# Kernel tuning notes

Measured on AMD Instinct MI355X. Metric: run time of the kernel, lower is better.

The kernel has to match this reference:

```python
import jax, jax.numpy as jnp
import numpy as np

B, L, IN, H, T = 512, 16, 128, 1024, 64


def setup_inputs() -> dict:
    key = jax.random.key(0)
    ks = jax.random.split(key, 11)
    k = 1.0 / np.sqrt(H)  # torch default init scale
    u = lambda kk, shape: jax.random.uniform(kk, shape, jnp.float32, -k, k)
    return {
        "x": jax.random.normal(ks[0], (B, L, IN), jnp.float32),
        "W_ih0": u(ks[1], (4 * H, IN)),
        "W_hh0": u(ks[2], (4 * H, H)),
        "b_ih0": u(ks[3], (4 * H,)),
        "b_hh0": u(ks[4], (4 * H,)),
        "W_ih1": u(ks[5], (4 * H, H)),
        "W_hh1": u(ks[6], (4 * H, H)),
        "b_ih1": u(ks[7], (4 * H,)),
        "b_hh1": u(ks[8], (4 * H,)),
        "W_out": u(ks[9], (IN, H)),
        "b_out": u(ks[10], (IN,)),
        "t": T,
    }


def _cell(xt, h, c, W_ih, W_hh, b_ih, b_hh):
    # PyTorch LSTM cell; gate order i, f, g, o
    g = xt @ W_ih.T + h @ W_hh.T + (b_ih + b_hh)
    i, f, gg, o = jnp.split(g, 4, axis=-1)
    c = jax.nn.sigmoid(f) * c + jax.nn.sigmoid(i) * jnp.tanh(gg)
    h = jax.nn.sigmoid(o) * jnp.tanh(c)
    return h, c


def reference(x, W_ih0, W_hh0, b_ih0, b_hh0, W_ih1, W_hh1, b_ih1, b_hh1,
              W_out, b_out, t):
    layers = ((W_ih0, W_hh0, b_ih0, b_hh0), (W_ih1, W_hh1, b_ih1, b_hh1))
    Bn = x.shape[0]
    Hn = W_hh0.shape[1]

    def stack_step(state, xt):
        new_state = []
        inp = xt
        for (h, c), p in zip(state, layers):
            h, c = _cell(inp, h, c, *p)
            new_state.append((h, c))
            inp = h
        return tuple(new_state), inp  # inp = top-layer hidden [B, H]

    z = jnp.zeros((Bn, Hn), x.dtype)
    state0 = tuple((z, z) for _ in layers)

    # prompt phase: process x over time, keep final state and last top hidden
    state, tops = jax.lax.scan(stack_step, state0, x.transpose(1, 0, 2))
    x_last = x[:, -1] + (tops[-1] @ W_out.T + b_out)  # [B, IN]

    def gen_step(carry, _):
        st, xl = carry
        st, htop = stack_step(st, xl)
        xl = xl + (htop @ W_out.T + b_out)
        return (st, xl), xl

    (_, _), gen = jax.lax.scan(gen_step, (state, x_last), None, length=t - 1)

    out = jnp.concatenate(
        [x, x_last[:, None, :], gen.transpose(1, 0, 2)], axis=1
    )  # [B, L + t, IN]
    return out
```

## Files before the change

### kernel.cpp

```cpp
#include <hip/hip_runtime.h>

#define B_    512
#define L_    16
#define IN_   128
#define H_    1024
#define T_    64
#define OUTROW 10240

#define LDC   1040
#define LDXL  144
#define RSTRIDE 67

#define KH_X  64
#define KH_H  32
#define KH_XL 4
#define KH_W0 36
#define KH_W1 64
#define KH_WO 32

typedef __attribute__((ext_vector_type(8))) short bf8;
typedef __attribute__((ext_vector_type(4))) float f4;
typedef __attribute__((ext_vector_type(4))) unsigned short us4;
typedef unsigned short u16;
typedef unsigned int   u32;

#define MFMA16(a, b, c) __builtin_amdgcn_mfma_f32_16x16x32_bf16(a, b, c, 0, 0, 0)

__device__ __forceinline__ u16 f2bf(float f) {
    u32 u = __builtin_bit_cast(u32, f);
    u32 r = (u + 0x7fffu + ((u >> 16) & 1u)) >> 16;
    return (u16)r;
}
__device__ __forceinline__ float sigm(float x) { return 1.f / (1.f + __expf(-x)); }
__device__ __forceinline__ float tanh_f(float x) {
    float ax = fabsf(x);
    float e = __expf(-2.f * ax);
    float t = (1.f - e) / (1.f + e);
    return x < 0.f ? -t : t;
}
__device__ __forceinline__ bf8 ld8(const u16* p) { return *(const bf8*)p; }

__device__ __forceinline__ size_t swz(int kh_stride, int row, int k) {
    return ((size_t)(row >> 4) * kh_stride + (k >> 5)) * 512
           + ((k & 31) >> 3) * 128 + (row & 15) * 8 + (k & 7);
}

#define MFMAT(AS, BS)                                                       \
  do {                                                                      \
    _Pragma("unroll")                                                       \
    for (int s_ = 0; s_ < 2; ++s_)                                          \
      _Pragma("unroll")                                                     \
      for (int g_ = 0; g_ < 4; ++g_)                                        \
        _Pragma("unroll")                                                   \
        for (int t_ = 0; t_ < 4; ++t_)                                      \
          acc[g_][t_] = MFMA16(AS[s_ * 4 + g_], BS[s_ * 4 + t_], acc[g_][t_]); \
  } while (0)

#define LOADT_CELL(AS, BS, KT)                                              \
  do {                                                                      \
    const int kt_ = (KT);                                                   \
    const bool ix_ = kt_ < nk1;                                             \
    const int khA_ = (ix_ ? kt_ : kt_ - nk1) * 2;                           \
    const int khB_ = kt_ * 2;                                               \
    _Pragma("unroll")                                                       \
    for (int s_ = 0; s_ < 2; ++s_) {                                        \
      _Pragma("unroll")                                                     \
      for (int g_ = 0; g_ < 4; ++g_)                                        \
        AS[s_ * 4 + g_] = ld8((ix_ ? apx[g_] : aph[g_]) + (khA_ + s_) * 512); \
      _Pragma("unroll")                                                     \
      for (int t_ = 0; t_ < 4; ++t_)                                        \
        BS[s_ * 4 + t_] = ld8(bp[t_] + (khB_ + s_) * 512);                  \
    }                                                                       \
  } while (0)

#define LOADT_PROJ(AS, BS, KT)                                              \
  do {                                                                      \
    const int kh_ = (KT) * 2;                                               \
    _Pragma("unroll")                                                       \
    for (int s_ = 0; s_ < 2; ++s_) {                                        \
      _Pragma("unroll")                                                     \
      for (int g_ = 0; g_ < 4; ++g_)                                        \
        AS[s_ * 4 + g_] = ld8(ap[g_] + (kh_ + s_) * 512);                   \
      _Pragma("unroll")                                                     \
      for (int t_ = 0; t_ < 4; ++t_)                                        \
        BS[s_ * 4 + t_] = ld8(bp[t_] + (kh_ + s_) * 512);                   \
    }                                                                       \
  } while (0)

__global__ __launch_bounds__(256, 2) void cell_gemm(
    const u16* __restrict__ pA0, int kh0, int nk1,
    const u16* __restrict__ pA1, int kh1, int nk2,
    const u16* __restrict__ pB, int khB,
    const float* __restrict__ bias, float* __restrict__ Cst, u16* __restrict__ Hdst)
{
    __shared__ float red[4][64 * RSTRIDE];
    const int bid = blockIdx.x;
    const int tn = (bid & 7) * 8 + ((bid >> 3) & 7);
    const int tm = bid >> 6;
    const int tid = threadIdx.x;
    const int lane = tid & 63, ws = tid >> 6;
    const int l15 = lane & 15, qd = lane >> 4, q4 = qd * 4;

    const int erow = ws * 16 + l15;
    const int grow = tm * 64 + erow;
    const int colb = tn * 16 + q4;
    const f4 cold = *(const f4*)&Cst[(size_t)grow * LDC + colb];

    f4 acc[4][4];
#pragma unroll
    for (int i = 0; i < 4; ++i)
#pragma unroll
        for (int j = 0; j < 4; ++j) acc[i][j] = (f4)(0.f);

    const u16* bp[4];
#pragma unroll
    for (int t = 0; t < 4; ++t)
        bp[t] = pB + (size_t)(tn * 4 + t) * khB * 512 + lane * 8;
    const u16* apx[4];
    const u16* aph[4];
#pragma unroll
    for (int g = 0; g < 4; ++g) {
        apx[g] = pA0 + (size_t)(tm * 4 + g) * kh0 * 512 + lane * 8;
        aph[g] = pA1 + (size_t)(tm * 4 + g) * kh1 * 512 + lane * 8;
    }

    const int nk  = nk1 + nk2;
    const int myn = (nk - ws + 3) >> 2;

    bf8 A0[8], B0[8], A1[8], B1[8];
    LOADT_CELL(A0, B0, ws);
    int i = 0, kt = ws;
    for (; i + 2 <= myn; i += 2, kt += 8) {
        LOADT_CELL(A1, B1, kt + 4);
        MFMAT(A0, B0);
        if (i + 2 < myn) LOADT_CELL(A0, B0, kt + 8);
        MFMAT(A1, B1);
    }
    if (i < myn) MFMAT(A0, B0);

#pragma unroll
    for (int rg = 0; rg < 4; ++rg)
#pragma unroll
        for (int t = 0; t < 4; ++t)
#pragma unroll
            for (int r = 0; r < 4; ++r)
                red[ws][(rg * 16 + q4 + r) * RSTRIDE + t * 16 + l15] = acc[rg][t][r];
    __syncthreads();

    f4 gs[4];
#pragma unroll
    for (int G = 0; G < 4; ++G) {
        f4 s;
#pragma unroll
        for (int j = 0; j < 4; ++j) {
            const int cidx = erow * RSTRIDE + G * 16 + q4 + j;
            s[j] = red[0][cidx] + red[1][cidx] + red[2][cidx] + red[3][cidx];
        }
        gs[G] = s + *(const f4*)&bias[tn * 64 + G * 16 + q4];
    }
    f4 cn; us4 h4;
#pragma unroll
    for (int j = 0; j < 4; ++j) {
        const float I  = sigm(gs[0][j]);
        const float F  = sigm(gs[1][j]);
        const float Gg = tanh_f(gs[2][j]);
        const float O  = sigm(gs[3][j]);
        cn[j] = F * cold[j] + I * Gg;
        h4[j] = f2bf(O * tanh_f(cn[j]));
    }
    *(f4*)&Cst[(size_t)grow * LDC + colb] = cn;
    *(us4*)&Hdst[swz(KH_H, grow, colb)] = h4;
}

__global__ __launch_bounds__(256, 2) void proj_gemm(
    const u16* __restrict__ pA,
    const u16* __restrict__ pB,
    const float* __restrict__ bout,
    const float* __restrict__ xin, int ldxin,
    float* __restrict__ XL, u16* __restrict__ XLbf,
    float* __restrict__ dout, int slot)
{
    __shared__ float red[4][64 * RSTRIDE];
    const int bid = blockIdx.x;
    const int tn = bid >> 3, tm = bid & 7;
    const int tid = threadIdx.x;
    const int lane = tid & 63, ws = tid >> 6;
    const int l15 = lane & 15, qd = lane >> 4;

    f4 acc[4][4];
#pragma unroll
    for (int i = 0; i < 4; ++i)
#pragma unroll
        for (int j = 0; j < 4; ++j) acc[i][j] = (f4)(0.f);

    const u16* bp[4];
#pragma unroll
    for (int t = 0; t < 4; ++t)
        bp[t] = pB + (size_t)(tn * 4 + t) * KH_WO * 512 + lane * 8;
    const u16* ap[4];
#pragma unroll
    for (int g = 0; g < 4; ++g)
        ap[g] = pA + (size_t)(tm * 4 + g) * KH_H * 512 + lane * 8;

    const int myn = 4;
    bf8 A0[8], B0[8], A1[8], B1[8];
    LOADT_PROJ(A0, B0, ws);
    int i = 0, kt = ws;
    for (; i + 2 <= myn; i += 2, kt += 8) {
        LOADT_PROJ(A1, B1, kt + 4);
        MFMAT(A0, B0);
        if (i + 2 < myn) LOADT_PROJ(A0, B0, kt + 8);
        MFMAT(A1, B1);
    }

#pragma unroll
    for (int rg = 0; rg < 4; ++rg)
#pragma unroll
        for (int t = 0; t < 4; ++t)
#pragma unroll
            for (int r = 0; r < 4; ++r)
                red[ws][(rg * 16 + qd * 4 + r) * RSTRIDE + t * 16 + l15] = acc[rg][t][r];
    __syncthreads();

    const int erow = ws * 16 + l15;
    const int grow = tm * 64 + erow;
#pragma unroll
    for (int jb = 0; jb < 4; ++jb) {
        const int cin = qd * 16 + jb * 4;
        const int col = tn * 64 + cin;
        f4 s;
#pragma unroll
        for (int j2 = 0; j2 < 4; ++j2) {
            const int cidx = erow * RSTRIDE + cin + j2;
            s[j2] = red[0][cidx] + red[1][cidx] + red[2][cidx] + red[3][cidx];
        }
        const f4 v = *(const f4*)&xin[(size_t)grow * ldxin + col] + s
                     + *(const f4*)&bout[col];
        *(f4*)&XL[(size_t)grow * LDXL + col] = v;
        us4 b;
#pragma unroll
        for (int j2 = 0; j2 < 4; ++j2) b[j2] = f2bf(v[j2]);
        *(us4*)&XLbf[swz(KH_XL, grow, col)] = b;
        *(f4*)&dout[(size_t)grow * OUTROW + slot * IN_ + col] = v;
    }
}

__global__ void conv_w(const float* Wih0, const float* Whh0, const float* bih0, const float* bhh0,
                       const float* Wih1, const float* Whh1, const float* bih1, const float* bhh1,
                       const float* Wout,
                       u16* W0c, float* b0p, u16* W1c, float* b1p, u16* Woutb)
{
    const int bid = blockIdx.x, t = threadIdx.x;
    const int lane = t >> 2;
    const int l15 = lane & 15, qd = lane >> 4;
    const int j0 = (t & 3) * 2;
    const int c0_ = qd * 8 + j0;

    if (bid < 9216) {
        const int rg = bid / 36, kh = bid - rg * 36;
        const int p = rg * 16 + l15;
        const int rem = p & 63, G = rem >> 4, u = (p >> 6) * 16 + (rem & 15);
        const int src = G * H_ + u;
        float e0, e1;
        if (kh < 4) {
            e0 = Wih0[(size_t)src * IN_ + kh * 32 + c0_];
            e1 = Wih0[(size_t)src * IN_ + kh * 32 + c0_ + 1];
        } else {
            e0 = Whh0[(size_t)src * H_ + (kh - 4) * 32 + c0_];
            e1 = Whh0[(size_t)src * H_ + (kh - 4) * 32 + c0_ + 1];
        }
        ((u32*)W0c)[(size_t)bid * 256 + t] = (u32)f2bf(e0) | ((u32)f2bf(e1) << 16);
        if (kh == 0 && qd == 0 && j0 == 0) b0p[p] = bih0[src] + bhh0[src];
    } else if (bid < 25600) {
        const int x = bid - 9216;
        const int rg = x >> 6, kh = x & 63;
        const int p = rg * 16 + l15;
        const int rem = p & 63, G = rem >> 4, u = (p >> 6) * 16 + (rem & 15);
        const int src = G * H_ + u;
        float e0, e1;
        if (kh < 32) {
            e0 = Wih1[(size_t)src * H_ + kh * 32 + c0_];
            e1 = Wih1[(size_t)src * H_ + kh * 32 + c0_ + 1];
        } else {
            e0 = Whh1[(size_t)src * H_ + (kh - 32) * 32 + c0_];
            e1 = Whh1[(size_t)src * H_ + (kh - 32) * 32 + c0_ + 1];
        }
        ((u32*)W1c)[(size_t)x * 256 + t] = (u32)f2bf(e0) | ((u32)f2bf(e1) << 16);
        if (kh == 0 && qd == 0 && j0 == 0) b1p[p] = bih1[src] + bhh1[src];
    } else {
        const int x = bid - 25600;
        const int rg = x >> 5, kh = x & 31;
        const int r = rg * 16 + l15;
        const float e0 = Wout[(size_t)r * H_ + kh * 32 + c0_];
        const float e1 = Wout[(size_t)r * H_ + kh * 32 + c0_ + 1];
        ((u32*)Woutb)[(size_t)x * 256 + t] = (u32)f2bf(e0) | ((u32)f2bf(e1) << 16);
    }
}

__global__ void setup_k(const float* __restrict__ x, u16* __restrict__ Xb,
                        u16* H0, u16* H1, float* c0, float* c1,
                        float* __restrict__ dout)
{
    const int i = blockIdx.x * 256 + threadIdx.x;
    const float v = x[i];
    const int r = i >> 11, col = i & 2047;
    Xb[swz(KH_X, r, col)] = f2bf(v);
    dout[(size_t)r * OUTROW + col] = v;
    if (i < B_ * H_) {
        H0[i] = 0; H1[i] = 0;
        const int rr = i >> 10, cc = i & 1023;
        c0[(size_t)rr * LDC + cc] = 0.f; c1[(size_t)rr * LDC + cc] = 0.f;
    }
}

extern "C" void kernel_launch(void* const* d_in, const int* in_sizes, int n_in,
                              void* d_out, int out_size, void* d_ws, size_t ws_size,
                              hipStream_t stream)
{
    const float* x    = (const float*)d_in[0];
    const float* Wih0 = (const float*)d_in[1];
    const float* Whh0 = (const float*)d_in[2];
    const float* bih0 = (const float*)d_in[3];
    const float* bhh0 = (const float*)d_in[4];
    const float* Wih1 = (const float*)d_in[5];
    const float* Whh1 = (const float*)d_in[6];
    const float* bih1 = (const float*)d_in[7];
    const float* bhh1 = (const float*)d_in[8];
    const float* Wout = (const float*)d_in[9];
    const float* bout = (const float*)d_in[10];
    float* dout = (float*)d_out;

    char* ws = (char*)d_ws;
    size_t off = 0;
    auto alloc = [&](size_t bytes) -> char* {
        char* p = ws + off; off += (bytes + 255) & ~(size_t)255; return p;
    };
    u16*  W0c   = (u16*)alloc((size_t)9216 * 1024);
    u16*  W1c   = (u16*)alloc((size_t)16384 * 1024);
    u16*  Woutb = (u16*)alloc((size_t)256 * 1024);
    float* b0p  = (float*)alloc(4096 * 4);
    float* b1p  = (float*)alloc(4096 * 4);
    u16*  Xb    = (u16*)alloc((size_t)2048 * 1024);
    u16*  H0b[2]; H0b[0] = (u16*)alloc((size_t)1024 * 1024); H0b[1] = (u16*)alloc((size_t)1024 * 1024);
    u16*  H1b[2]; H1b[0] = (u16*)alloc((size_t)1024 * 1024); H1b[1] = (u16*)alloc((size_t)1024 * 1024);
    float* c0   = (float*)alloc((size_t)B_ * LDC * 4);
    float* c1   = (float*)alloc((size_t)B_ * LDC * 4);
    float* XL   = (float*)alloc((size_t)B_ * LDXL * 4);
    u16*  XLbf  = (u16*)alloc((size_t)128 * 1024);

    conv_w<<<25856, 256, 0, stream>>>(Wih0, Whh0, bih0, bhh0,
                                      Wih1, Whh1, bih1, bhh1, Wout,
                                      W0c, b0p, W1c, b1p, Woutb);
    setup_k<<<4096, 256, 0, stream>>>(x, Xb, H0b[0], H1b[0], c0, c1, dout);

    int p = 0;
    for (int g = 0; g < 79; ++g) {
        const u16* xpart; int khx;
        if (g < 16) { xpart = Xb + (size_t)g * 2048; khx = KH_X; }
        else        { xpart = XLbf;                  khx = KH_XL; }
        cell_gemm<<<512, 256, 0, stream>>>(xpart, khx, 2, H0b[p], KH_H, 16,
                                           W0c, KH_W0, b0p, c0, H0b[1 - p]);
        cell_gemm<<<512, 256, 0, stream>>>(H0b[1 - p], KH_H, 16, H1b[p], KH_H, 16,
                                           W1c, KH_W1, b1p, c1, H1b[1 - p]);
        if (g >= 15) {
            const int s = g - 15;
            const float* xin; int ldxin;
            if (s == 0) { xin = x + 15 * IN_; ldxin = L_ * IN_; }
            else        { xin = XL;           ldxin = LDXL; }
            proj_gemm<<<16, 256, 0, stream>>>(H1b[1 - p], Woutb, bout,
                                              xin, ldxin, XL, XLbf, dout, 16 + s);
        }
        p ^= 1;
    }
}
```

Measured before the change: 2.676 ms.

## Wavefront-pair prompt LSTM layers and widen cell blocks to eight waves

During the prompt phase, layer 1 at step g and layer 0 at step g+1 are independent, so they now run as one combined launch of 1024 blocks. This doubles the parallelism per launch and cuts the launch count. Cell and projection kernels move to 512 threads (8 waves splitting K), with template-specialised strides. The LDS reduction runs in two rounds with a per-element epilogue. The software double-buffered register prefetch is removed, which relies on higher occupancy to hide memory latency, and the reduction now has more LDS traffic and an extra barrier.

```diff
diff --git a/kernel.cpp b/kernel.cpp
--- a/kernel.cpp
+++ b/kernel.cpp
@@ -9,7 +9,7 @@
 
 #define LDC   1040
 #define LDXL  144
-#define RSTRIDE 67
+#define RST   68
 
 #define KH_X  64
 #define KH_H  32
@@ -45,201 +45,195 @@
            + ((k & 31) >> 3) * 128 + (row & 15) * 8 + (k & 7);
 }
 
-#define MFMAT(AS, BS)                                                       \
-  do {                                                                      \
-    _Pragma("unroll")                                                       \
-    for (int s_ = 0; s_ < 2; ++s_)                                          \
-      _Pragma("unroll")                                                     \
-      for (int g_ = 0; g_ < 4; ++g_)                                        \
-        _Pragma("unroll")                                                   \
-        for (int t_ = 0; t_ < 4; ++t_)                                      \
-          acc[g_][t_] = MFMA16(AS[s_ * 4 + g_], BS[s_ * 4 + t_], acc[g_][t_]); \
-  } while (0)
-
-#define LOADT_CELL(AS, BS, KT)                                              \
-  do {                                                                      \
-    const int kt_ = (KT);                                                   \
-    const bool ix_ = kt_ < nk1;                                             \
-    const int khA_ = (ix_ ? kt_ : kt_ - nk1) * 2;                           \
-    const int khB_ = kt_ * 2;                                               \
-    _Pragma("unroll")                                                       \
-    for (int s_ = 0; s_ < 2; ++s_) {                                        \
-      _Pragma("unroll")                                                     \
-      for (int g_ = 0; g_ < 4; ++g_)                                        \
-        AS[s_ * 4 + g_] = ld8((ix_ ? apx[g_] : aph[g_]) + (khA_ + s_) * 512); \
-      _Pragma("unroll")                                                     \
-      for (int t_ = 0; t_ < 4; ++t_)                                        \
-        BS[s_ * 4 + t_] = ld8(bp[t_] + (khB_ + s_) * 512);                  \
-    }                                                                       \
-  } while (0)
-
-#define LOADT_PROJ(AS, BS, KT)                                              \
-  do {                                                                      \
-    const int kh_ = (KT) * 2;                                               \
-    _Pragma("unroll")                                                       \
-    for (int s_ = 0; s_ < 2; ++s_) {                                        \
-      _Pragma("unroll")                                                     \
-      for (int g_ = 0; g_ < 4; ++g_)                                        \
-        AS[s_ * 4 + g_] = ld8(ap[g_] + (kh_ + s_) * 512);                   \
-      _Pragma("unroll")                                                     \
-      for (int t_ = 0; t_ < 4; ++t_)                                        \
-        BS[s_ * 4 + t_] = ld8(bp[t_] + (kh_ + s_) * 512);                   \
-    }                                                                       \
-  } while (0)
-
-__global__ __launch_bounds__(256, 2) void cell_gemm(
-    const u16* __restrict__ pA0, int kh0, int nk1,
-    const u16* __restrict__ pA1, int kh1, int nk2,
-    const u16* __restrict__ pB, int khB,
-    const float* __restrict__ bias, float* __restrict__ Cst, u16* __restrict__ Hdst)
-{
-    __shared__ float red[4][64 * RSTRIDE];
-    const int bid = blockIdx.x;
+template<int KH0, int NK1, int KH1, int NK2, int KHB>
+__device__ __forceinline__ void gemm_loop(f4 (&acc)[4][4], int tm, int tn,
+    int lane, int ws,
+    const u16* __restrict__ pA0, const u16* __restrict__ pA1,
+    const u16* __restrict__ pB)
+{
+#pragma unroll
+    for (int i = 0; i < 4; ++i)
+#pragma unroll
+        for (int j = 0; j < 4; ++j) acc[i][j] = (f4)(0.f);
+
+    const int lo = lane * 8;
+    const int nk  = NK1 + NK2;
+    const int myn = (nk - ws + 7) >> 3;
+
+    bf8 A[4], B[4];
+    for (int m = 0; m < myn; ++m) {
+        const int kt = ws + m * 8;
+        const bool ix = kt < NK1;
+        const int khA = (ix ? kt : kt - NK1) * 2;
+        const int khB = kt * 2;
+        const u16* ap = ix ? pA0 : pA1;
+        const int khs = ix ? KH0 : KH1;
+#pragma unroll
+        for (int s = 0; s < 2; ++s) {
+#pragma unroll
+            for (int g = 0; g < 4; ++g)
+                A[g] = ld8(ap + ((size_t)(tm * 4 + g) * khs + khA + s) * 512 + lo);
+#pragma unroll
+            for (int t = 0; t < 4; ++t)
+                B[t] = ld8(pB + ((size_t)(tn * 4 + t) * KHB + khB + s) * 512 + lo);
+#pragma unroll
+            for (int g = 0; g < 4; ++g)
+#pragma unroll
+                for (int t = 0; t < 4; ++t)
+                    acc[g][t] = MFMA16(A[g], B[t], acc[g][t]);
+        }
+    }
+}
+
+template<int KH0, int NK1, int KH1, int NK2, int KHB>
+__device__ __forceinline__ void cell_body(int bid,
+    const u16* __restrict__ pA0, const u16* __restrict__ pA1,
+    const u16* __restrict__ pB, const float* __restrict__ bias,
+    float* __restrict__ Cst, u16* __restrict__ Hdst, float* red)
+{
     const int tn = (bid & 7) * 8 + ((bid >> 3) & 7);
     const int tm = bid >> 6;
     const int tid = threadIdx.x;
     const int lane = tid & 63, ws = tid >> 6;
-    const int l15 = lane & 15, qd = lane >> 4, q4 = qd * 4;
-
-    const int erow = ws * 16 + l15;
-    const int grow = tm * 64 + erow;
-    const int colb = tn * 16 + q4;
-    const f4 cold = *(const f4*)&Cst[(size_t)grow * LDC + colb];
+    const int l15 = lane & 15, qd = lane >> 4;
+
+    const int eu = tid & 15, elr = tid >> 4;
+    const int ecol = tn * 16 + eu;
+    const float cold0 = Cst[(size_t)(tm * 64 + elr) * LDC + ecol];
+    const float cold1 = Cst[(size_t)(tm * 64 + 32 + elr) * LDC + ecol];
+    f4 bi;
+#pragma unroll
+    for (int G = 0; G < 4; ++G) bi[G] = bias[tn * 64 + G * 16 + eu];
 
     f4 acc[4][4];
-#pragma unroll
-    for (int i = 0; i < 4; ++i)
-#pragma unroll
-        for (int j = 0; j < 4; ++j) acc[i][j] = (f4)(0.f);
-
-    const u16* bp[4];
-#pragma unroll
-    for (int t = 0; t < 4; ++t)
-        bp[t] = pB + (size_t)(tn * 4 + t) * khB * 512 + lane * 8;
-    const u16* apx[4];
-    const u16* aph[4];
-#pragma unroll
-    for (int g = 0; g < 4; ++g) {
-        apx[g] = pA0 + (size_t)(tm * 4 + g) * kh0 * 512 + lane * 8;
-        aph[g] = pA1 + (size_t)(tm * 4 + g) * kh1 * 512 + lane * 8;
-    }
-
-    const int nk  = nk1 + nk2;
-    const int myn = (nk - ws + 3) >> 2;
-
-    bf8 A0[8], B0[8], A1[8], B1[8];
-    LOADT_CELL(A0, B0, ws);
-    int i = 0, kt = ws;
-    for (; i + 2 <= myn; i += 2, kt += 8) {
-        LOADT_CELL(A1, B1, kt + 4);
-        MFMAT(A0, B0);
-        if (i + 2 < myn) LOADT_CELL(A0, B0, kt + 8);
-        MFMAT(A1, B1);
-    }
-    if (i < myn) MFMAT(A0, B0);
-
-#pragma unroll
-    for (int rg = 0; rg < 4; ++rg)
-#pragma unroll
-        for (int t = 0; t < 4; ++t)
-#pragma unroll
-            for (int r = 0; r < 4; ++r)
-                red[ws][(rg * 16 + q4 + r) * RSTRIDE + t * 16 + l15] = acc[rg][t][r];
-    __syncthreads();
-
-    f4 gs[4];
-#pragma unroll
-    for (int G = 0; G < 4; ++G) {
-        f4 s;
-#pragma unroll
-        for (int j = 0; j < 4; ++j) {
-            const int cidx = erow * RSTRIDE + G * 16 + q4 + j;
-            s[j] = red[0][cidx] + red[1][cidx] + red[2][cidx] + red[3][cidx];
-        }
-        gs[G] = s + *(const f4*)&bias[tn * 64 + G * 16 + q4];
-    }
-    f4 cn; us4 h4;
-#pragma unroll
-    for (int j = 0; j < 4; ++j) {
-        const float I  = sigm(gs[0][j]);
-        const float F  = sigm(gs[1][j]);
-        const float Gg = tanh_f(gs[2][j]);
-        const float O  = sigm(gs[3][j]);
-        cn[j] = F * cold[j] + I * Gg;
-        h4[j] = f2bf(O * tanh_f(cn[j]));
-    }
-    *(f4*)&Cst[(size_t)grow * LDC + colb] = cn;
-    *(us4*)&Hdst[swz(KH_H, grow, colb)] = h4;
-}
-
-__global__ __launch_bounds__(256, 2) void proj_gemm(
-    const u16* __restrict__ pA,
-    const u16* __restrict__ pB,
+    gemm_loop<KH0, NK1, KH1, NK2, KHB>(acc, tm, tn, lane, ws, pA0, pA1, pB);
+
+#pragma unroll
+    for (int round = 0; round < 2; ++round) {
+        if (round) __syncthreads();
+#pragma unroll
+        for (int rh = 0; rh < 2; ++rh) {
+            const int rg = round * 2 + rh;
+#pragma unroll
+            for (int t = 0; t < 4; ++t)
+#pragma unroll
+                for (int r = 0; r < 4; ++r)
+                    red[ws * (32 * RST) + (rh * 16 + qd * 4 + r) * RST + t * 16 + l15]
+                        = acc[rg][t][r];
+        }
+        __syncthreads();
+
+        float g4[4];
+#pragma unroll
+        for (int G = 0; G < 4; ++G) {
+            float s = 0.f;
+#pragma unroll
+            for (int w = 0; w < 8; ++w)
+                s += red[w * (32 * RST) + elr * RST + G * 16 + eu];
+            g4[G] = s + bi[G];
+        }
+        const float I  = sigm(g4[0]);
+        const float F  = sigm(g4[1]);
+        const float Gg = tanh_f(g4[2]);
+        const float O  = sigm(g4[3]);
+        const int grow = tm * 64 + round * 32 + elr;
+        const float cn = F * (round ? cold1 : cold0) + I * Gg;
+        Cst[(size_t)grow * LDC + ecol] = cn;
+        Hdst[swz(KH_H, grow, ecol)] = f2bf(O * tanh_f(cn));
+    }
+}
+
+__global__ __launch_bounds__(512, 4) void cell_prompt0(
+    const u16* __restrict__ pA0, const u16* __restrict__ pA1,
+    const u16* __restrict__ pB, const float* __restrict__ bias,
+    float* __restrict__ Cst, u16* __restrict__ Hdst)
+{
+    __shared__ float red[8 * 32 * RST];
+    cell_body<KH_X, 2, KH_H, 16, KH_W0>(blockIdx.x, pA0, pA1, pB, bias, Cst, Hdst, red);
+}
+
+__global__ __launch_bounds__(512, 4) void cell_roll0(
+    const u16* __restrict__ pA0, const u16* __restrict__ pA1,
+    const u16* __restrict__ pB, const float* __restrict__ bias,
+    float* __restrict__ Cst, u16* __restrict__ Hdst)
+{
+    __shared__ float red[8 * 32 * RST];
+    cell_body<KH_XL, 2, KH_H, 16, KH_W0>(blockIdx.x, pA0, pA1, pB, bias, Cst, Hdst, red);
+}
+
+__global__ __launch_bounds__(512, 4) void cell_l1(
+    const u16* __restrict__ pA0, const u16* __restrict__ pA1,
+    const u16* __restrict__ pB, const float* __restrict__ bias,
+    float* __restrict__ Cst, u16* __restrict__ Hdst)
+{
+    __shared__ float red[8 * 32 * RST];
+    cell_body<KH_H, 16, KH_H, 16, KH_W1>(blockIdx.x, pA0, pA1, pB, bias, Cst, Hdst, red);
+}
+
+__global__ __launch_bounds__(512, 4) void pair_k(
+    const u16* __restrict__ A0a, const u16* __restrict__ A1a,
+    const u16* __restrict__ Ba, const float* __restrict__ ba,
+    float* __restrict__ Ca, u16* __restrict__ Ha,
+    const u16* __restrict__ A0b, const u16* __restrict__ A1b,
+    const u16* __restrict__ Bb, const float* __restrict__ bb,
+    float* __restrict__ Cb, u16* __restrict__ Hb)
+{
+    __shared__ float red[8 * 32 * RST];
+    if (blockIdx.x < 512)
+        cell_body<KH_H, 16, KH_H, 16, KH_W1>(blockIdx.x, A0a, A1a, Ba, ba, Ca, Ha, red);
+    else
+        cell_body<KH_X, 2, KH_H, 16, KH_W0>(blockIdx.x - 512, A0b, A1b, Bb, bb, Cb, Hb, red);
+}
+
+__global__ __launch_bounds__(512, 4) void proj_gemm(
+    const u16* __restrict__ pA, const u16* __restrict__ pB,
     const float* __restrict__ bout,
     const float* __restrict__ xin, int ldxin,
     float* __restrict__ XL, u16* __restrict__ XLbf,
     float* __restrict__ dout, int slot)
 {
-    __shared__ float red[4][64 * RSTRIDE];
+    __shared__ float red[8 * 32 * RST];
     const int bid = blockIdx.x;
     const int tn = bid >> 3, tm = bid & 7;
     const int tid = threadIdx.x;
     const int lane = tid & 63, ws = tid >> 6;
     const int l15 = lane & 15, qd = lane >> 4;
 
+    const int elr = tid >> 4;
+    const int c4  = (tid & 15) * 4;
+    const int col = tn * 64 + c4;
+    const f4 bo  = *(const f4*)&bout[col];
+    const f4 xv0 = *(const f4*)&xin[(size_t)(tm * 64 + elr) * ldxin + col];
+    const f4 xv1 = *(const f4*)&xin[(size_t)(tm * 64 + 32 + elr) * ldxin + col];
+
     f4 acc[4][4];
-#pragma unroll
-    for (int i = 0; i < 4; ++i)
-#pragma unroll
-        for (int j = 0; j < 4; ++j) acc[i][j] = (f4)(0.f);
-
-    const u16* bp[4];
-#pragma unroll
-    for (int t = 0; t < 4; ++t)
-        bp[t] = pB + (size_t)(tn * 4 + t) * KH_WO * 512 + lane * 8;
-    const u16* ap[4];
-#pragma unroll
-    for (int g = 0; g < 4; ++g)
-        ap[g] = pA + (size_t)(tm * 4 + g) * KH_H * 512 + lane * 8;
-
-    const int myn = 4;
-    bf8 A0[8], B0[8], A1[8], B1[8];
-    LOADT_PROJ(A0, B0, ws);
-    int i = 0, kt = ws;
-    for (; i + 2 <= myn; i += 2, kt += 8) {
-        LOADT_PROJ(A1, B1, kt + 4);
-        MFMAT(A0, B0);
-        if (i + 2 < myn) LOADT_PROJ(A0, B0, kt + 8);
-        MFMAT(A1, B1);
-    }
-
-#pragma unroll
-    for (int rg = 0; rg < 4; ++rg)
-#pragma unroll
-        for (int t = 0; t < 4; ++t)
-#pragma unroll
-            for (int r = 0; r < 4; ++r)
-                red[ws][(rg * 16 + qd * 4 + r) * RSTRIDE + t * 16 + l15] = acc[rg][t][r];
-    __syncthreads();
-
-    const int erow = ws * 16 + l15;
-    const int grow = tm * 64 + erow;
-#pragma unroll
-    for (int jb = 0; jb < 4; ++jb) {
-        const int cin = qd * 16 + jb * 4;
-        const int col = tn * 64 + cin;
-        f4 s;
-#pragma unroll
-        for (int j2 = 0; j2 < 4; ++j2) {
-            const int cidx = erow * RSTRIDE + cin + j2;
-            s[j2] = red[0][cidx] + red[1][cidx] + red[2][cidx] + red[3][cidx];
-        }
-        const f4 v = *(const f4*)&xin[(size_t)grow * ldxin + col] + s
-                     + *(const f4*)&bout[col];
+    gemm_loop<KH_H, 16, KH_H, 0, KH_WO>(acc, tm, tn, lane, ws, pA, pA, pB);
+
+#pragma unroll
+    for (int round = 0; round < 2; ++round) {
+        if (round) __syncthreads();
+#pragma unroll
+        for (int rh = 0; rh < 2; ++rh) {
+            const int rg = round * 2 + rh;
+#pragma unroll
+            for (int t = 0; t < 4; ++t)
+#pragma unroll
+                for (int r = 0; r < 4; ++r)
+                    red[ws * (32 * RST) + (rh * 16 + qd * 4 + r) * RST + t * 16 + l15]
+                        = acc[rg][t][r];
+        }
+        __syncthreads();
+
+        f4 s = (f4)(0.f);
+#pragma unroll
+        for (int w = 0; w < 8; ++w)
+            s += *(const f4*)&red[w * (32 * RST) + elr * RST + c4];
+        const f4 v = (round ? xv1 : xv0) + s + bo;
+        const int grow = tm * 64 + round * 32 + elr;
         *(f4*)&XL[(size_t)grow * LDXL + col] = v;
         us4 b;
 #pragma unroll
-        for (int j2 = 0; j2 < 4; ++j2) b[j2] = f2bf(v[j2]);
+        for (int j = 0; j < 4; ++j) b[j] = f2bf(v[j]);
         *(us4*)&XLbf[swz(KH_XL, grow, col)] = b;
         *(f4*)&dout[(size_t)grow * OUTROW + slot * IN_ + col] = v;
     }
@@ -354,22 +348,24 @@
     setup_k<<<4096, 256, 0, stream>>>(x, Xb, H0b[0], H1b[0], c0, c1, dout);
 
     int p = 0;
-    for (int g = 0; g < 79; ++g) {
-        const u16* xpart; int khx;
-        if (g < 16) { xpart = Xb + (size_t)g * 2048; khx = KH_X; }
-        else        { xpart = XLbf;                  khx = KH_XL; }
-        cell_gemm<<<512, 256, 0, stream>>>(xpart, khx, 2, H0b[p], KH_H, 16,
-                                           W0c, KH_W0, b0p, c0, H0b[1 - p]);
-        cell_gemm<<<512, 256, 0, stream>>>(H0b[1 - p], KH_H, 16, H1b[p], KH_H, 16,
-                                           W1c, KH_W1, b1p, c1, H1b[1 - p]);
-        if (g >= 15) {
-            const int s = g - 15;
-            const float* xin; int ldxin;
-            if (s == 0) { xin = x + 15 * IN_; ldxin = L_ * IN_; }
-            else        { xin = XL;           ldxin = LDXL; }
-            proj_gemm<<<16, 256, 0, stream>>>(H1b[1 - p], Woutb, bout,
-                                              xin, ldxin, XL, XLbf, dout, 16 + s);
-        }
+    cell_prompt0<<<512, 512, 0, stream>>>(Xb, H0b[0], W0c, b0p, c0, H0b[1]);
+    for (int g = 0; g < 15; ++g) {
+        pair_k<<<1024, 512, 0, stream>>>(
+            H0b[1 - p], H1b[p], W1c, b1p, c1, H1b[1 - p],
+            Xb + (size_t)(g + 1) * 2048, H0b[1 - p], W0c, b0p, c0, H0b[p]);
         p ^= 1;
     }
-}
+    cell_l1<<<512, 512, 0, stream>>>(H0b[0], H1b[1], W1c, b1p, c1, H1b[0]);
+    proj_gemm<<<16, 512, 0, stream>>>(H1b[0], Woutb, bout,
+                                      x + 15 * IN_, L_ * IN_, XL, XLbf, dout, 16);
+
+    p = 0;
+    for (int g = 16; g < 79; ++g) {
+        cell_roll0<<<512, 512, 0, stream>>>(XLbf, H0b[p], W0c, b0p, c0, H0b[1 - p]);
+        cell_l1<<<512, 512, 0, stream>>>(H0b[1 - p], H1b[p], W1c, b1p, c1, H1b[1 - p]);
+        const int s = g - 15;
+        proj_gemm<<<16, 512, 0, stream>>>(H1b[1 - p], Woutb, bout,
+                                          XL, LDXL, XL, XLbf, dout, 16 + s);
+        p ^= 1;
+    }
+}
```

Result: slower. 3.490 ms (+30.4%).

## Wavefront-pair layer0/layer1 cells in prompt phase and deepen load pipeline

Applied to the files above, without the earlier changes.

During the 16-step prompt phase, layer-1 at step t and layer-0 at step t+1 are independent, so they are fused into one 1024-block launch (pair_k). This halves the number of dependent launches in that phase and fills more CUs per launch. Separately, the GEMM inner loops are restructured from a two-stage double buffer of 8-fragment tiles into a four-stage ring of 4-fragment half-tiles, adding prefetch depth at similar register cost. The H buffer ping-pong indexing is rearranged to match the skewed schedule, which carries some correctness risk.

```diff
diff --git a/kernel.cpp b/kernel.cpp
--- a/kernel.cpp
+++ b/kernel.cpp
@@ -10,6 +10,7 @@
 #define LDC   1040
 #define LDXL  144
 #define RSTRIDE 67
+#define RSZ   (64 * RSTRIDE)
 
 #define KH_X  64
 #define KH_H  32
@@ -45,56 +46,46 @@
            + ((k & 31) >> 3) * 128 + (row & 15) * 8 + (k & 7);
 }
 
-#define MFMAT(AS, BS)                                                       \
+#define MFMAP(AS, BS)                                                       \
   do {                                                                      \
     _Pragma("unroll")                                                       \
-    for (int s_ = 0; s_ < 2; ++s_)                                          \
-      _Pragma("unroll")                                                     \
-      for (int g_ = 0; g_ < 4; ++g_)                                        \
-        _Pragma("unroll")                                                   \
-        for (int t_ = 0; t_ < 4; ++t_)                                      \
-          acc[g_][t_] = MFMA16(AS[s_ * 4 + g_], BS[s_ * 4 + t_], acc[g_][t_]); \
-  } while (0)
-
-#define LOADT_CELL(AS, BS, KT)                                              \
-  do {                                                                      \
-    const int kt_ = (KT);                                                   \
-    const bool ix_ = kt_ < nk1;                                             \
-    const int khA_ = (ix_ ? kt_ : kt_ - nk1) * 2;                           \
-    const int khB_ = kt_ * 2;                                               \
-    _Pragma("unroll")                                                       \
-    for (int s_ = 0; s_ < 2; ++s_) {                                        \
-      _Pragma("unroll")                                                     \
-      for (int g_ = 0; g_ < 4; ++g_)                                        \
-        AS[s_ * 4 + g_] = ld8((ix_ ? apx[g_] : aph[g_]) + (khA_ + s_) * 512); \
+    for (int g_ = 0; g_ < 4; ++g_)                                          \
       _Pragma("unroll")                                                     \
       for (int t_ = 0; t_ < 4; ++t_)                                        \
-        BS[s_ * 4 + t_] = ld8(bp[t_] + (khB_ + s_) * 512);                  \
-    }                                                                       \
+        acc[g_][t_] = MFMA16(AS[g_], BS[t_], acc[g_][t_]);                  \
   } while (0)
 
-#define LOADT_PROJ(AS, BS, KT)                                              \
+#define LOADP_CELL(AS, BS, PH)                                              \
   do {                                                                      \
-    const int kh_ = (KT) * 2;                                               \
+    const int kt_ = ws + (((PH) >> 1) << 2);                                \
+    const int s_  = (PH) & 1;                                               \
+    const bool ix_ = kt_ < nk1;                                             \
+    const int oA_ = (((ix_ ? kt_ : kt_ - nk1) << 1) + s_) * 512;            \
+    const int oB_ = ((kt_ << 1) + s_) * 512;                                \
     _Pragma("unroll")                                                       \
-    for (int s_ = 0; s_ < 2; ++s_) {                                        \
-      _Pragma("unroll")                                                     \
-      for (int g_ = 0; g_ < 4; ++g_)                                        \
-        AS[s_ * 4 + g_] = ld8(ap[g_] + (kh_ + s_) * 512);                   \
-      _Pragma("unroll")                                                     \
-      for (int t_ = 0; t_ < 4; ++t_)                                        \
-        BS[s_ * 4 + t_] = ld8(bp[t_] + (kh_ + s_) * 512);                   \
-    }                                                                       \
+    for (int g_ = 0; g_ < 4; ++g_)                                          \
+      AS[g_] = ld8((ix_ ? apx[g_] : aph[g_]) + oA_);                        \
+    _Pragma("unroll")                                                       \
+    for (int t_ = 0; t_ < 4; ++t_) BS[t_] = ld8(bp[t_] + oB_);              \
   } while (0)
 
-__global__ __launch_bounds__(256, 2) void cell_gemm(
+#define LOADP_PROJ(AS, BS, PH)                                              \
+  do {                                                                      \
+    const int kt_ = ws + (((PH) >> 1) << 2);                                \
+    const int o_  = ((kt_ << 1) + ((PH) & 1)) * 512;                        \
+    _Pragma("unroll")                                                       \
+    for (int g_ = 0; g_ < 4; ++g_) AS[g_] = ld8(ap[g_] + o_);               \
+    _Pragma("unroll")                                                       \
+    for (int t_ = 0; t_ < 4; ++t_) BS[t_] = ld8(bp[t_] + o_);               \
+  } while (0)
+
+__device__ __forceinline__ void cell_body(int bid,
     const u16* __restrict__ pA0, int kh0, int nk1,
     const u16* __restrict__ pA1, int kh1, int nk2,
     const u16* __restrict__ pB, int khB,
-    const float* __restrict__ bias, float* __restrict__ Cst, u16* __restrict__ Hdst)
-{
-    __shared__ float red[4][64 * RSTRIDE];
-    const int bid = blockIdx.x;
+    const float* __restrict__ bias, float* __restrict__ Cst,
+    u16* __restrict__ Hdst, float* __restrict__ red)
+{
     const int tn = (bid & 7) * 8 + ((bid >> 3) & 7);
     const int tm = bid >> 6;
     const int tid = threadIdx.x;
@@ -126,17 +117,27 @@
 
     const int nk  = nk1 + nk2;
     const int myn = (nk - ws + 3) >> 2;
-
-    bf8 A0[8], B0[8], A1[8], B1[8];
-    LOADT_CELL(A0, B0, ws);
-    int i = 0, kt = ws;
-    for (; i + 2 <= myn; i += 2, kt += 8) {
-        LOADT_CELL(A1, B1, kt + 4);
-        MFMAT(A0, B0);
-        if (i + 2 < myn) LOADT_CELL(A0, B0, kt + 8);
-        MFMAT(A1, B1);
-    }
-    if (i < myn) MFMAT(A0, B0);
+    const int nph = myn * 2;
+
+    bf8 A0[4], B0[4], A1[4], B1[4], A2[4], B2[4], A3[4], B3[4];
+    LOADP_CELL(A0, B0, 0);
+    LOADP_CELL(A1, B1, 1);
+    LOADP_CELL(A2, B2, 2);
+    int ph = 0;
+    for (; ph + 4 <= nph; ph += 4) {
+        LOADP_CELL(A3, B3, ph + 3);
+        MFMAP(A0, B0);
+        if (ph + 4 < nph) LOADP_CELL(A0, B0, ph + 4);
+        MFMAP(A1, B1);
+        if (ph + 5 < nph) LOADP_CELL(A1, B1, ph + 5);
+        MFMAP(A2, B2);
+        if (ph + 6 < nph) LOADP_CELL(A2, B2, ph + 6);
+        MFMAP(A3, B3);
+    }
+    if (ph < nph) {
+        MFMAP(A0, B0);
+        MFMAP(A1, B1);
+    }
 
 #pragma unroll
     for (int rg = 0; rg < 4; ++rg)
@@ -144,7 +145,7 @@
         for (int t = 0; t < 4; ++t)
 #pragma unroll
             for (int r = 0; r < 4; ++r)
-                red[ws][(rg * 16 + q4 + r) * RSTRIDE + t * 16 + l15] = acc[rg][t][r];
+                red[ws * RSZ + (rg * 16 + q4 + r) * RSTRIDE + t * 16 + l15] = acc[rg][t][r];
     __syncthreads();
 
     f4 gs[4];
@@ -154,7 +155,8 @@
 #pragma unroll
         for (int j = 0; j < 4; ++j) {
             const int cidx = erow * RSTRIDE + G * 16 + q4 + j;
-            s[j] = red[0][cidx] + red[1][cidx] + red[2][cidx] + red[3][cidx];
+            s[j] = red[0 * RSZ + cidx] + red[1 * RSZ + cidx]
+                 + red[2 * RSZ + cidx] + red[3 * RSZ + cidx];
         }
         gs[G] = s + *(const f4*)&bias[tn * 64 + G * 16 + q4];
     }
@@ -172,6 +174,33 @@
     *(us4*)&Hdst[swz(KH_H, grow, colb)] = h4;
 }
 
+__global__ __launch_bounds__(256, 2) void cell_gemm(
+    const u16* __restrict__ pA0, int kh0, int nk1,
+    const u16* __restrict__ pA1, int kh1, int nk2,
+    const u16* __restrict__ pB, int khB,
+    const float* __restrict__ bias, float* __restrict__ Cst, u16* __restrict__ Hdst)
+{
+    __shared__ float red[4 * RSZ];
+    cell_body(blockIdx.x, pA0, kh0, nk1, pA1, kh1, nk2, pB, khB, bias, Cst, Hdst, red);
+}
+
+__global__ __launch_bounds__(256, 2) void pair_k(
+    const u16* __restrict__ A0a, int kh0a, int nk1a,
+    const u16* __restrict__ A1a, int kh1a, int nk2a,
+    const u16* __restrict__ Ba, int khBa,
+    const float* __restrict__ ba, float* __restrict__ Ca, u16* __restrict__ Ha,
+    const u16* __restrict__ A0b, int kh0b, int nk1b,
+    const u16* __restrict__ A1b, int kh1b, int nk2b,
+    const u16* __restrict__ Bb, int khBb,
+    const float* __restrict__ bb, float* __restrict__ Cb, u16* __restrict__ Hb)
+{
+    __shared__ float red[4 * RSZ];
+    if (blockIdx.x < 512)
+        cell_body(blockIdx.x, A0a, kh0a, nk1a, A1a, kh1a, nk2a, Ba, khBa, ba, Ca, Ha, red);
+    else
+        cell_body(blockIdx.x - 512, A0b, kh0b, nk1b, A1b, kh1b, nk2b, Bb, khBb, bb, Cb, Hb, red);
+}
+
 __global__ __launch_bounds__(256, 2) void proj_gemm(
     const u16* __restrict__ pA,
     const u16* __restrict__ pB,
@@ -180,7 +209,7 @@
     float* __restrict__ XL, u16* __restrict__ XLbf,
     float* __restrict__ dout, int slot)
 {
-    __shared__ float red[4][64 * RSTRIDE];
+    __shared__ float red[4 * RSZ];
     const int bid = blockIdx.x;
     const int tn = bid >> 3, tm = bid & 7;
     const int tid = threadIdx.x;
@@ -202,15 +231,20 @@
     for (int g = 0; g < 4; ++g)
         ap[g] = pA + (size_t)(tm * 4 + g) * KH_H * 512 + lane * 8;
 
-    const int myn = 4;
-    bf8 A0[8], B0[8], A1[8], B1[8];
-    LOADT_PROJ(A0, B0, ws);
-    int i = 0, kt = ws;
-    for (; i + 2 <= myn; i += 2, kt += 8) {
-        LOADT_PROJ(A1, B1, kt + 4);
-        MFMAT(A0, B0);
-        if (i + 2 < myn) LOADT_PROJ(A0, B0, kt + 8);
-        MFMAT(A1, B1);
+    const int nph = 8;
+    bf8 A0[4], B0[4], A1[4], B1[4], A2[4], B2[4], A3[4], B3[4];
+    LOADP_PROJ(A0, B0, 0);
+    LOADP_PROJ(A1, B1, 1);
+    LOADP_PROJ(A2, B2, 2);
+    for (int ph = 0; ph + 4 <= nph; ph += 4) {
+        LOADP_PROJ(A3, B3, ph + 3);
+        MFMAP(A0, B0);
+        if (ph + 4 < nph) LOADP_PROJ(A0, B0, ph + 4);
+        MFMAP(A1, B1);
+        if (ph + 5 < nph) LOADP_PROJ(A1, B1, ph + 5);
+        MFMAP(A2, B2);
+        if (ph + 6 < nph) LOADP_PROJ(A2, B2, ph + 6);
+        MFMAP(A3, B3);
     }
 
 #pragma unroll
@@ -219,7 +253,7 @@
         for (int t = 0; t < 4; ++t)
 #pragma unroll
             for (int r = 0; r < 4; ++r)
-                red[ws][(rg * 16 + qd * 4 + r) * RSTRIDE + t * 16 + l15] = acc[rg][t][r];
+                red[ws * RSZ + (rg * 16 + qd * 4 + r) * RSTRIDE + t * 16 + l15] = acc[rg][t][r];
     __syncthreads();
 
     const int erow = ws * 16 + l15;
@@ -232,7 +266,8 @@
 #pragma unroll
         for (int j2 = 0; j2 < 4; ++j2) {
             const int cidx = erow * RSTRIDE + cin + j2;
-            s[j2] = red[0][cidx] + red[1][cidx] + red[2][cidx] + red[3][cidx];
+            s[j2] = red[0 * RSZ + cidx] + red[1 * RSZ + cidx]
+                  + red[2 * RSZ + cidx] + red[3 * RSZ + cidx];
         }
         const f4 v = *(const f4*)&xin[(size_t)grow * ldxin + col] + s
                      + *(const f4*)&bout[col];
@@ -354,22 +389,29 @@
     setup_k<<<4096, 256, 0, stream>>>(x, Xb, H0b[0], H1b[0], c0, c1, dout);
 
     int p = 0;
-    for (int g = 0; g < 79; ++g) {
-        const u16* xpart; int khx;
-        if (g < 16) { xpart = Xb + (size_t)g * 2048; khx = KH_X; }
-        else        { xpart = XLbf;                  khx = KH_XL; }
-        cell_gemm<<<512, 256, 0, stream>>>(xpart, khx, 2, H0b[p], KH_H, 16,
+    cell_gemm<<<512, 256, 0, stream>>>(Xb, KH_X, 2, H0b[0], KH_H, 16,
+                                       W0c, KH_W0, b0p, c0, H0b[1]);
+    for (int g = 0; g < 15; ++g) {
+        pair_k<<<1024, 256, 0, stream>>>(
+            H0b[1 - p], KH_H, 16, H1b[p], KH_H, 16, W1c, KH_W1, b1p, c1, H1b[1 - p],
+            Xb + (size_t)(g + 1) * 2048, KH_X, 2, H0b[1 - p], KH_H, 16,
+            W0c, KH_W0, b0p, c0, H0b[p]);
+        p ^= 1;
+    }
+    cell_gemm<<<512, 256, 0, stream>>>(H0b[0], KH_H, 16, H1b[1], KH_H, 16,
+                                       W1c, KH_W1, b1p, c1, H1b[0]);
+    proj_gemm<<<16, 256, 0, stream>>>(H1b[0], Woutb, bout,
+                                      x + 15 * IN_, L_ * IN_, XL, XLbf, dout, 16);
+
+    p = 0;
+    for (int g = 16; g < 79; ++g) {
+        cell_gemm<<<512, 256, 0, stream>>>(XLbf, KH_XL, 2, H0b[p], KH_H, 16,
                                            W0c, KH_W0, b0p, c0, H0b[1 - p]);
         cell_gemm<<<512, 256, 0, stream>>>(H0b[1 - p], KH_H, 16, H1b[p], KH_H, 16,
                                            W1c, KH_W1, b1p, c1, H1b[1 - p]);
-        if (g >= 15) {
-            const int s = g - 15;
-            const float* xin; int ldxin;
-            if (s == 0) { xin = x + 15 * IN_; ldxin = L_ * IN_; }
-            else        { xin = XL;           ldxin = LDXL; }
-            proj_gemm<<<16, 256, 0, stream>>>(H1b[1 - p], Woutb, bout,
-                                              xin, ldxin, XL, XLbf, dout, 16 + s);
-        }
+        const int s = g - 15;
+        proj_gemm<<<16, 256, 0, stream>>>(H1b[1 - p], Woutb, bout,
+                                          XL, LDXL, XL, XLbf, dout, 16 + s);
         p ^= 1;
     }
 }
```

Result: faster. 2.623 ms (-2.0%).
